# Optimization experiments

Hardware: AMD Instinct MI355X
Metric: run time of the kernel (lower is better)

The kernel has to match this reference:

```python
import jax, jax.numpy as jnp
import numpy as np

N_NODES = 2_000_000
E = 1_000_000
MEM = 32      # memory_dim
MSG = 32      # message_dim
EMB = 32      # embed_dim
EDGE = 2      # edge_dim


def _linear_params(key, out_dim, in_dim):
    kw, kb = jax.random.split(key)
    bound = 1.0 / np.sqrt(in_dim)
    W = jax.random.uniform(kw, (out_dim, in_dim), jnp.float32, -bound, bound)
    b = jax.random.uniform(kb, (out_dim,), jnp.float32, -bound, bound)
    return W, b


def setup_inputs() -> dict:
    key = jax.random.key(0)
    ks = jax.random.split(key, 16)
    inp = {}
    inp["src_ids"] = jax.random.randint(ks[0], (E,), 0, N_NODES)
    inp["dst_ids"] = jax.random.randint(ks[1], (E,), 0, N_NODES)
    inp["edge_feat"] = jax.random.normal(ks[2], (E, EDGE), jnp.float32)
    inp["delta_t"] = jax.random.uniform(ks[3], (E, 1), jnp.float32)
    # persistent node memory (torch init is zeros; use randn for a non-trivial baseline)
    inp["memory"] = jax.random.normal(ks[4], (N_NODES, MEM), jnp.float32) * 0.1
    # MessageFunction MLP: (2*MEM + EDGE + 1) -> MSG -> MSG
    inp["msg_W1"], inp["msg_b1"] = _linear_params(ks[5], MSG, 2 * MEM + EDGE + 1)
    inp["msg_W2"], inp["msg_b2"] = _linear_params(ks[6], MSG, MSG)
    # GRUCell(MSG, MEM): weight_ih [3*MEM, MSG], weight_hh [3*MEM, MEM]
    inp["gru_w_ih"], inp["gru_b_ih"] = _linear_params(ks[7], 3 * MEM, MSG)
    inp["gru_w_hh"], inp["gru_b_hh"] = _linear_params(ks[8], 3 * MEM, MEM)
    # MultiheadAttention with seq_len=1: only V and out projections affect output
    inp["attn_Wv"], inp["attn_bv"] = _linear_params(ks[9], MEM, MEM)
    inp["attn_Wo"], inp["attn_bo"] = _linear_params(ks[10], MEM, MEM)
    # TemporalEmbedding MLP: (MEM + EDGE) -> EMB -> EMB
    inp["emb_W1"], inp["emb_b1"] = _linear_params(ks[11], EMB, MEM + EDGE)
    inp["emb_W2"], inp["emb_b2"] = _linear_params(ks[12], EMB, EMB)
    # AnomalyClassifier: EMB -> 32 -> 1
    inp["cls_W1"], inp["cls_b1"] = _linear_params(ks[13], 32, EMB)
    inp["cls_W2"], inp["cls_b2"] = _linear_params(ks[14], 1, 32)
    return inp


def reference(src_ids, dst_ids, edge_feat, delta_t, memory,
              msg_W1, msg_b1, msg_W2, msg_b2,
              gru_w_ih, gru_w_hh, gru_b_ih, gru_b_hh,
              attn_Wv, attn_bv, attn_Wo, attn_bo,
              emb_W1, emb_b1, emb_W2, emb_b2,
              cls_W1, cls_b1, cls_W2, cls_b2):
    # gather per-node memory  [E, MEM]
    src_mem = memory[src_ids]
    dst_mem = memory[dst_ids]

    # MessageFunction: concat + 2-layer MLP
    x = jnp.concatenate([src_mem, dst_mem, edge_feat, delta_t], axis=-1)  # [E, 67]
    h = jax.nn.relu(x @ msg_W1.T + msg_b1)
    msg = h @ msg_W2.T + msg_b2  # [E, MSG]

    # GRUCell update on dst memory (torch gate order: r, z, n)
    gi = msg @ gru_w_ih.T + gru_b_ih      # [E, 3*MEM]
    gh = dst_mem @ gru_w_hh.T + gru_b_hh  # [E, 3*MEM]
    i_r, i_z, i_n = jnp.split(gi, 3, axis=-1)
    h_r, h_z, h_n = jnp.split(gh, 3, axis=-1)
    r = jax.nn.sigmoid(i_r + h_r)
    z = jax.nn.sigmoid(i_z + h_z)
    n = jnp.tanh(i_n + r * h_n)
    updated = (1.0 - z) * n + z * dst_mem  # [E, MEM]
    # scatter back into persistent buffer (detached in the torch module)
    new_memory = memory.at[dst_ids].set(jax.lax.stop_gradient(updated))

    # TemporalEmbedding: self-attention over a length-1 sequence. softmax of a
    # single score is exactly 1, so attn_out == out_proj(v_proj(dst_mem)).
    attn_out = (dst_mem @ attn_Wv.T + attn_bv) @ attn_Wo.T + attn_bo  # [E, MEM]
    e = jnp.concatenate([attn_out, edge_feat], axis=-1)  # [E, MEM+EDGE]
    embed = jax.nn.relu(e @ emb_W1.T + emb_b1) @ emb_W2.T + emb_b2  # [E, EMB]

    # AnomalyClassifier (dropout is identity at eval)
    logits = jax.nn.relu(embed @ cls_W1.T + cls_b1) @ cls_W2.T + cls_b2  # [E, 1]
    probs = jax.nn.sigmoid(logits).squeeze(-1)  # [E]
    return probs, new_memory
```

## Files before the change

### kernel.cpp

```cpp
#include <hip/hip_runtime.h>
#include <hip/hip_bf16.h>

typedef float  f32x4v __attribute__((ext_vector_type(4)));
typedef short  bf16x8 __attribute__((ext_vector_type(8)));

#define NFRAG   26
#define TB_F32  512
#define FRG_U16 (NFRAG*512)
#define SHARE_BYTES (TB_F32*4 + FRG_U16*2)
#define SHARE_U4 (SHARE_BYTES/16)
#define WC_OFF 7168

#define BLK 256
#define COPY_BLOCKS 256
#define EDGE_BLOCKS 1024
#define GRID (COPY_BLOCKS + EDGE_BLOCKS)
#define EDGE_WAVES (EDGE_BLOCKS * 4)

#define MFMA(a,b,c) __builtin_amdgcn_mfma_f32_16x16x32_bf16(a,b,c,0,0,0)

__device__ __forceinline__ float sigf(float v) { return 1.0f / (1.0f + __expf(-v)); }
__device__ __forceinline__ float tanhf_fast(float v) {
    float a = fabsf(v);
    float t = __expf(-2.0f * a);
    float r = (1.0f - t) / (1.0f + t);
    return v < 0.0f ? -r : r;
}
__device__ __forceinline__ unsigned pk(float a, float b) {
    union { __hip_bfloat162 h; unsigned u; } c;
    c.h = __float22bfloat162_rn(make_float2(a, b));
    return c.u;
}

union FragU { uint4 u4; bf16x8 s8; unsigned u[4]; };

__device__ __forceinline__ bf16x8 ldfrag(const unsigned short* frg, int idx_u16) {
    FragU c; c.u4 = *(const uint4*)(frg + idx_u16); return c.s8;
}
__device__ __forceinline__ f32x4v tbl(const float* tb, int idx_f32) {
    return *(const f32x4v*)(tb + idx_f32);
}
__device__ __forceinline__ bf16x8 relayout_reg(f32x4v h0, f32x4v h1) {
    FragU c;
    c.u[0] = pk(h0[0], h0[1]); c.u[1] = pk(h0[2], h0[3]);
    c.u[2] = pk(h1[0], h1[1]); c.u[3] = pk(h1[2], h1[3]);
    return c.s8;
}

__global__ void winner_k(const int* __restrict__ dst_ids, int* __restrict__ winner, int E) {
    int e = blockIdx.x * 256 + threadIdx.x;
    if (e < E) atomicMax(winner + dst_ids[e], e + 1);
}

__global__ void prep_k(const float* __restrict__ msg_W1, const float* __restrict__ msg_b1,
                       const float* __restrict__ msg_W2, const float* __restrict__ msg_b2,
                       const float* __restrict__ w_ih, const float* __restrict__ b_ih,
                       const float* __restrict__ w_hh, const float* __restrict__ b_hh,
                       const float* __restrict__ Wv, const float* __restrict__ bv,
                       const float* __restrict__ Wo, const float* __restrict__ bo,
                       const float* __restrict__ emb_W1, const float* __restrict__ emb_b1,
                       const float* __restrict__ emb_W2, const float* __restrict__ emb_b2,
                       const float* __restrict__ cls_W1, const float* __restrict__ cls_b1,
                       const float* __restrict__ cls_W2, float* __restrict__ WSf) {
    int t = threadIdx.x;
    float* tb = WSf;
    unsigned short* frg = (unsigned short*)(WSf + TB_F32);
    float* WC = WSf + WC_OFF;
    if (t < 32) {
        int j = t;
        tb[0*32+j]  = msg_b1[j];
        tb[1*32+j]  = msg_W1[j*67+64];
        tb[2*32+j]  = msg_W1[j*67+65];
        tb[3*32+j]  = msg_W1[j*67+66];
        tb[4*32+j]  = msg_b2[j];
        tb[5*32+j]  = b_ih[32+j] + b_hh[32+j];
        tb[6*32+j]  = b_ih[j] + b_hh[j];
        tb[7*32+j]  = b_hh[64+j];
        tb[8*32+j]  = b_ih[64+j];
        float a = bo[j];
        for (int o = 0; o < 32; ++o) a += Wo[j*32+o] * bv[o];
        tb[9*32+j]  = a;
        tb[10*32+j] = emb_b1[j];
        tb[11*32+j] = emb_W1[j*34+32];
        tb[12*32+j] = emb_W1[j*34+33];
        tb[13*32+j] = emb_b2[j];
        tb[14*32+j] = cls_b1[j];
        tb[15*32+j] = cls_W2[j];
    }
    for (int i = t; i < 1024; i += 256) {
        int j = i >> 5, k = i & 31;
        float a = 0.0f;
        for (int o = 0; o < 32; ++o) a += Wo[j*32+o] * Wv[o*32+k];
        WC[i] = a;
    }
    __syncthreads();
    for (int idx = t; idx < NFRAG * 512; idx += 256) {
        int f = idx >> 9, l = (idx >> 3) & 63, i = idx & 7;
        int r = l & 15, kb = ((l >> 4) << 3) + i;
        const float* P; int j0 = 0, k0 = 0, ld = 32;
        bool mapped = false;
        switch (f) {
            case 0:  P = msg_W1; j0 = 0;  k0 = 0;  ld = 67; break;
            case 1:  P = msg_W1; j0 = 0;  k0 = 32; ld = 67; break;
            case 2:  P = msg_W1; j0 = 16; k0 = 0;  ld = 67; break;
            case 3:  P = msg_W1; j0 = 16; k0 = 32; ld = 67; break;
            case 4:  P = msg_W2; j0 = 0;  mapped = true; break;
            case 5:  P = msg_W2; j0 = 16; mapped = true; break;
            case 6:  P = w_ih;   j0 = 32; mapped = true; break;
            case 7:  P = w_hh;   j0 = 32; break;
            case 8:  P = w_ih;   j0 = 48; mapped = true; break;
            case 9:  P = w_hh;   j0 = 48; break;
            case 10: P = w_ih;   j0 = 0;  mapped = true; break;
            case 11: P = w_hh;   j0 = 0;  break;
            case 12: P = w_ih;   j0 = 16; mapped = true; break;
            case 13: P = w_hh;   j0 = 16; break;
            case 14: P = w_hh;   j0 = 64; break;
            case 15: P = w_hh;   j0 = 80; break;
            case 16: P = w_ih;   j0 = 64; mapped = true; break;
            case 17: P = w_ih;   j0 = 80; mapped = true; break;
            case 18: P = WC;     j0 = 0;  break;
            case 19: P = WC;     j0 = 16; break;
            case 20: P = emb_W1; j0 = 0;  ld = 34; mapped = true; break;
            case 21: P = emb_W1; j0 = 16; ld = 34; mapped = true; break;
            case 22: P = emb_W2; j0 = 0;  mapped = true; break;
            case 23: P = emb_W2; j0 = 16; mapped = true; break;
            case 24: P = cls_W1; j0 = 0;  mapped = true; break;
            default: P = cls_W1; j0 = 16; mapped = true; break;
        }
        int kidx = kb;
        if (mapped) kidx = 16 * ((kb >> 2) & 1) + 4 * (kb >> 3) + (kb & 3);
        __hip_bfloat16 hv = __float2bfloat16(P[(j0 + r) * ld + k0 + kidx]);
        frg[idx] = *(unsigned short*)&hv;
    }
}

__device__ __forceinline__ void compute16(
    int grp, int E, int eI, int g, int lane,
    int e, int dst, int winv, float2 ef, float dtv,
    f32x4v sa, f32x4v sb, f32x4v da, f32x4v db, f32x4v t0, f32x4v t1,
    const float* tb, const unsigned short* frg, float clsb2,
    float* __restrict__ probs, float* __restrict__ out_mem) {
    int ob = 0, tbo = 0;
    asm volatile("" : "+v"(ob), "+v"(tbo));

    FragU Bs, Bd;
    Bs.u[0] = pk(sa[0], sa[1]); Bs.u[1] = pk(sa[2], sa[3]);
    Bs.u[2] = pk(sb[0], sb[1]); Bs.u[3] = pk(sb[2], sb[3]);
    Bd.u[0] = pk(da[0], da[1]); Bd.u[1] = pk(da[2], da[3]);
    Bd.u[2] = pk(db[0], db[1]); Bd.u[3] = pk(db[2], db[3]);
    f32x4v dmt[2]; dmt[0] = t0; dmt[1] = t1;

    f32x4v h[2];
#pragma unroll
    for (int jt = 0; jt < 2; ++jt) {
        f32x4v b1v = tbl(tb, 0*32 + jt*16 + 4*g + tbo);
        f32x4v w64 = tbl(tb, 1*32 + jt*16 + 4*g + tbo);
        f32x4v w65 = tbl(tb, 2*32 + jt*16 + 4*g + tbo);
        f32x4v w66 = tbl(tb, 3*32 + jt*16 + 4*g + tbo);
        f32x4v c;
#pragma unroll
        for (int i = 0; i < 4; ++i)
            c[i] = b1v[i] + ef.x * w64[i] + ef.y * w65[i] + dtv * w66[i];
        c = MFMA(ldfrag(frg, (jt*2+1)*512 + lane*8 + ob), Bd.s8, c);
        c = MFMA(ldfrag(frg, (jt*2+0)*512 + lane*8 + ob), Bs.s8, c);
#pragma unroll
        for (int i = 0; i < 4; ++i) c[i] = fmaxf(c[i], 0.0f);
        h[jt] = c;
    }
    bf16x8 Bh = relayout_reg(h[0], h[1]);

    f32x4v m[2];
#pragma unroll
    for (int jt = 0; jt < 2; ++jt)
        m[jt] = MFMA(ldfrag(frg, (4+jt)*512 + lane*8 + ob), Bh,
                     tbl(tb, 4*32 + jt*16 + 4*g + tbo));
    bf16x8 Bm = relayout_reg(m[0], m[1]);

    f32x4v zz[2], uu[2];
#pragma unroll
    for (int jt = 0; jt < 2; ++jt) {
        f32x4v c = tbl(tb, 5*32 + jt*16 + 4*g + tbo);
        c = MFMA(ldfrag(frg, (7+2*jt)*512 + lane*8 + ob), Bd.s8, c);
        c = MFMA(ldfrag(frg, (6+2*jt)*512 + lane*8 + ob), Bm, c);
#pragma unroll
        for (int i = 0; i < 4; ++i) c[i] = sigf(c[i]);
        zz[jt] = c;
    }
#pragma unroll
    for (int jt = 0; jt < 2; ++jt) {
        f32x4v c = tbl(tb, 6*32 + jt*16 + 4*g + tbo);
        c = MFMA(ldfrag(frg, (11+2*jt)*512 + lane*8 + ob), Bd.s8, c);
        c = MFMA(ldfrag(frg, (10+2*jt)*512 + lane*8 + ob), Bm, c);
        f32x4v hn = tbl(tb, 7*32 + jt*16 + 4*g + tbo);
        hn = MFMA(ldfrag(frg, (14+jt)*512 + lane*8 + ob), Bd.s8, hn);
        f32x4v bin = tbl(tb, 8*32 + jt*16 + 4*g + tbo);
        f32x4v npre;
#pragma unroll
        for (int i = 0; i < 4; ++i) npre[i] = fmaf(sigf(c[i]), hn[i], bin[i]);
        npre = MFMA(ldfrag(frg, (16+jt)*512 + lane*8 + ob), Bm, npre);
#pragma unroll
        for (int i = 0; i < 4; ++i) {
            float n = tanhf_fast(npre[i]);
            uu[jt][i] = n + zz[jt][i] * (dmt[jt][i] - n);
        }
    }
    if (winv == e + 1) {
        f32x4v* orow = (f32x4v*)(out_mem + (size_t)dst * 32);
        orow[g]     = uu[0];
        orow[4 + g] = uu[1];
    }

    f32x4v at[2];
#pragma unroll
    for (int jt = 0; jt < 2; ++jt)
        at[jt] = MFMA(ldfrag(frg, (18+jt)*512 + lane*8 + ob), Bd.s8,
                      tbl(tb, 9*32 + jt*16 + 4*g + tbo));
    bf16x8 Ba = relayout_reg(at[0], at[1]);
    f32x4v e1v[2];
#pragma unroll
    for (int jt = 0; jt < 2; ++jt) {
        f32x4v b  = tbl(tb, 10*32 + jt*16 + 4*g + tbo);
        f32x4v wa = tbl(tb, 11*32 + jt*16 + 4*g + tbo);
        f32x4v wb = tbl(tb, 12*32 + jt*16 + 4*g + tbo);
        f32x4v c;
#pragma unroll
        for (int i = 0; i < 4; ++i) c[i] = b[i] + ef.x * wa[i] + ef.y * wb[i];
        c = MFMA(ldfrag(frg, (20+jt)*512 + lane*8 + ob), Ba, c);
#pragma unroll
        for (int i = 0; i < 4; ++i) c[i] = fmaxf(c[i], 0.0f);
        e1v[jt] = c;
    }
    bf16x8 B1 = relayout_reg(e1v[0], e1v[1]);
    f32x4v e2v[2];
#pragma unroll
    for (int jt = 0; jt < 2; ++jt)
        e2v[jt] = MFMA(ldfrag(frg, (22+jt)*512 + lane*8 + ob), B1,
                       tbl(tb, 13*32 + jt*16 + 4*g + tbo));
    bf16x8 B2 = relayout_reg(e2v[0], e2v[1]);
    float part = 0.0f;
#pragma unroll
    for (int jt = 0; jt < 2; ++jt) {
        f32x4v c = MFMA(ldfrag(frg, (24+jt)*512 + lane*8 + ob), B2,
                        tbl(tb, 14*32 + jt*16 + 4*g + tbo));
        f32x4v w2 = tbl(tb, 15*32 + jt*16 + 4*g + tbo);
#pragma unroll
        for (int i = 0; i < 4; ++i) part = fmaf(fmaxf(c[i], 0.0f), w2[i], part);
    }
    part += __shfl_xor(part, 16);
    part += __shfl_xor(part, 32);
    if (lane < 16) {
        int ee = grp * 16 + eI;
        if (ee < E) probs[ee] = sigf(part + clsb2);
    }
}

__global__ __launch_bounds__(BLK, 5) void tgn_mfma16(
    const int* __restrict__ src_ids, const int* __restrict__ dst_ids,
    const float* __restrict__ edge_feat, const float* __restrict__ delta_t,
    const float* __restrict__ memory, const float* __restrict__ cls_b2,
    const float* __restrict__ WSf, const int* __restrict__ winner,
    float* __restrict__ probs, float* __restrict__ out_mem,
    int E, int N, int ngrp) {
    __shared__ uint4 sbuf[SHARE_U4];
    int bid = blockIdx.x, tid = threadIdx.x;

    if (bid < COPY_BLOCKS) {
        const f32x4v* m4 = (const f32x4v*)memory;
        f32x4v* o4 = (f32x4v*)out_mem;
        const long S = (long)COPY_BLOCKS * BLK;
        const long total4 = (long)N * 8;
        long i0 = (long)bid * BLK + tid;
        for (; i0 + 3 * S < total4; i0 += 4 * S) {
            long i1 = i0 + S, i2 = i0 + 2 * S, i3 = i0 + 3 * S;
            int w0 = winner[i0 >> 3];
            int w1 = winner[i1 >> 3];
            int w2 = winner[i2 >> 3];
            int w3 = winner[i3 >> 3];
            if (w0 == 0) o4[i0] = m4[i0];
            if (w1 == 0) o4[i1] = m4[i1];
            if (w2 == 0) o4[i2] = m4[i2];
            if (w3 == 0) o4[i3] = m4[i3];
        }
        for (; i0 < total4; i0 += S) {
            if (winner[i0 >> 3] == 0) o4[i0] = m4[i0];
        }
        return;
    }

    {
        const uint4* s = (const uint4*)WSf;
        for (int i = tid; i < SHARE_U4; i += BLK) sbuf[i] = s[i];
    }
    __syncthreads();
    const float* tb = (const float*)sbuf;
    const unsigned short* frg = (const unsigned short*)((const float*)sbuf + TB_F32);
    int wv = tid >> 6, lane = tid & 63;
    int eI = lane & 15, g = lane >> 4;
    int ewid = (bid - COPY_BLOCKS) * 4 + wv;
    float clsb2 = cls_b2[0];

#define PREF(P, G) do {                                                              \
    int ee = (G) * 16 + eI; if (ee >= E) ee = E - 1;                                 \
    e##P = ee;                                                                       \
    int sid = src_ids[ee]; dst##P = dst_ids[ee];                                     \
    ef##P = ((const float2*)edge_feat)[ee]; dt##P = delta_t[ee];                     \
    win##P = winner[dst##P];                                                         \
    const f32x4v* sp_ = (const f32x4v*)(memory + (size_t)sid * 32);                  \
    const f32x4v* dp_ = (const f32x4v*)(memory + (size_t)dst##P * 32);               \
    S##P##a = sp_[2*g]; S##P##b = sp_[2*g+1];                                        \
    D##P##a = dp_[2*g]; D##P##b = dp_[2*g+1];                                        \
    T##P##0 = dp_[g];   T##P##1 = dp_[4+g];                                          \
} while (0)

    int g0 = ewid;
    if (g0 < ngrp) {
        int eA, dstA, winA; float2 efA; float dtA;
        f32x4v SAa, SAb, DAa, DAb, TA0, TA1;
        int eB, dstB, winB; float2 efB; float dtB;
        f32x4v SBa, SBb, DBa, DBb, TB0, TB1;
        PREF(A, g0);
        for (;;) {
            int gn = g0 + EDGE_WAVES;
            { int gp = (gn < ngrp) ? gn : (ngrp - 1); PREF(B, gp); }
            asm volatile("" ::: "memory");
            compute16(g0, E, eI, g, lane, eA, dstA, winA, efA, dtA,
                      SAa, SAb, DAa, DAb, TA0, TA1,
                      tb, frg, clsb2, probs, out_mem);
            if (gn >= ngrp) break;
            g0 = gn;
            gn = g0 + EDGE_WAVES;
            { int gp = (gn < ngrp) ? gn : (ngrp - 1); PREF(A, gp); }
            asm volatile("" ::: "memory");
            compute16(g0, E, eI, g, lane, eB, dstB, winB, efB, dtB,
                      SBa, SBb, DBa, DBb, TB0, TB1,
                      tb, frg, clsb2, probs, out_mem);
            if (gn >= ngrp) break;
            g0 = gn;
        }
    }
#undef PREF
}

extern "C" void kernel_launch(void* const* d_in, const int* in_sizes, int n_in,
                              void* d_out, int out_size, void* d_ws, size_t ws_size,
                              hipStream_t stream) {
    const int*   src_ids   = (const int*)d_in[0];
    const int*   dst_ids   = (const int*)d_in[1];
    const float* edge_feat = (const float*)d_in[2];
    const float* delta_t   = (const float*)d_in[3];
    const float* memory    = (const float*)d_in[4];
    const float* msg_W1 = (const float*)d_in[5],  *msg_b1 = (const float*)d_in[6];
    const float* msg_W2 = (const float*)d_in[7],  *msg_b2 = (const float*)d_in[8];
    const float* w_ih   = (const float*)d_in[9],  *b_ih   = (const float*)d_in[10];
    const float* w_hh   = (const float*)d_in[11], *b_hh   = (const float*)d_in[12];
    const float* Wv     = (const float*)d_in[13], *bv     = (const float*)d_in[14];
    const float* Wo     = (const float*)d_in[15], *bo     = (const float*)d_in[16];
    const float* emb_W1 = (const float*)d_in[17], *emb_b1 = (const float*)d_in[18];
    const float* emb_W2 = (const float*)d_in[19], *emb_b2 = (const float*)d_in[20];
    const float* cls_W1 = (const float*)d_in[21], *cls_b1 = (const float*)d_in[22];
    const float* cls_W2 = (const float*)d_in[23], *cls_b2 = (const float*)d_in[24];

    int E = in_sizes[0];
    int N = in_sizes[4] / 32;
    int ngrp = (E + 15) / 16;

    int*   winner = (int*)d_ws;
    float* WSf    = (float*)((char*)d_ws + (size_t)N * sizeof(int));
    float* probs  = (float*)d_out;
    float* outmem = probs + E;

    hipMemsetAsync(winner, 0, (size_t)N * sizeof(int), stream);
    winner_k<<<(E + 255) / 256, 256, 0, stream>>>(dst_ids, winner, E);
    prep_k<<<1, 256, 0, stream>>>(msg_W1, msg_b1, msg_W2, msg_b2,
                                  w_ih, b_ih, w_hh, b_hh,
                                  Wv, bv, Wo, bo,
                                  emb_W1, emb_b1, emb_W2, emb_b2,
                                  cls_W1, cls_b1, cls_W2, WSf);
    tgn_mfma16<<<GRID, BLK, 0, stream>>>(src_ids, dst_ids, edge_feat, delta_t,
                                         memory, cls_b2, WSf, winner,
                                         probs, outmem, E, N, ngrp);
}
```

Before: 298.8 us.

## Interleave independent MFMA chains, split weight prep, use fast reciprocals

The per-tile compute is reordered so the GRU, attention/embedding and classifier MFMA chains are interleaved, letting independent matrix ops hide each other's latency. Weight-fragment packing moves into a separate kernel with one block per fragment instead of a single block. Sigmoid and tanh divisions become hardware reciprocals. Edge block count and launch-bounds occupancy are lowered, which gives more registers per thread but fewer waves to hide memory latency.

After: 279.4 us. 6.5% less time.

```diff
diff --git a/kernel.cpp b/kernel.cpp
--- a/kernel.cpp
+++ b/kernel.cpp
@@ -13,17 +13,19 @@
 
 #define BLK 256
 #define COPY_BLOCKS 256
-#define EDGE_BLOCKS 1024
+#define EDGE_BLOCKS 768
 #define GRID (COPY_BLOCKS + EDGE_BLOCKS)
 #define EDGE_WAVES (EDGE_BLOCKS * 4)
 
 #define MFMA(a,b,c) __builtin_amdgcn_mfma_f32_16x16x32_bf16(a,b,c,0,0,0)
 
-__device__ __forceinline__ float sigf(float v) { return 1.0f / (1.0f + __expf(-v)); }
+__device__ __forceinline__ float sigf(float v) {
+    return __builtin_amdgcn_rcpf(1.0f + __expf(-v));
+}
 __device__ __forceinline__ float tanhf_fast(float v) {
     float a = fabsf(v);
     float t = __expf(-2.0f * a);
-    float r = (1.0f - t) / (1.0f + t);
+    float r = (1.0f - t) * __builtin_amdgcn_rcpf(1.0f + t);
     return v < 0.0f ? -r : r;
 }
 __device__ __forceinline__ unsigned pk(float a, float b) {
@@ -52,19 +54,17 @@
     if (e < E) atomicMax(winner + dst_ids[e], e + 1);
 }
 
-__global__ void prep_k(const float* __restrict__ msg_W1, const float* __restrict__ msg_b1,
-                       const float* __restrict__ msg_W2, const float* __restrict__ msg_b2,
-                       const float* __restrict__ w_ih, const float* __restrict__ b_ih,
-                       const float* __restrict__ w_hh, const float* __restrict__ b_hh,
-                       const float* __restrict__ Wv, const float* __restrict__ bv,
-                       const float* __restrict__ Wo, const float* __restrict__ bo,
-                       const float* __restrict__ emb_W1, const float* __restrict__ emb_b1,
-                       const float* __restrict__ emb_W2, const float* __restrict__ emb_b2,
-                       const float* __restrict__ cls_W1, const float* __restrict__ cls_b1,
-                       const float* __restrict__ cls_W2, float* __restrict__ WSf) {
+__global__ void prep_wc_k(const float* __restrict__ msg_W1, const float* __restrict__ msg_b1,
+                          const float* __restrict__ msg_b2,
+                          const float* __restrict__ b_ih, const float* __restrict__ b_hh,
+                          const float* __restrict__ Wv, const float* __restrict__ bv,
+                          const float* __restrict__ Wo, const float* __restrict__ bo,
+                          const float* __restrict__ emb_W1, const float* __restrict__ emb_b1,
+                          const float* __restrict__ emb_b2,
+                          const float* __restrict__ cls_b1, const float* __restrict__ cls_W2,
+                          float* __restrict__ WSf) {
     int t = threadIdx.x;
     float* tb = WSf;
-    unsigned short* frg = (unsigned short*)(WSf + TB_F32);
     float* WC = WSf + WC_OFF;
     if (t < 32) {
         int j = t;
@@ -93,9 +93,21 @@
         for (int o = 0; o < 32; ++o) a += Wo[j*32+o] * Wv[o*32+k];
         WC[i] = a;
     }
-    __syncthreads();
-    for (int idx = t; idx < NFRAG * 512; idx += 256) {
-        int f = idx >> 9, l = (idx >> 3) & 63, i = idx & 7;
+}
+
+__global__ void prep_frag_k(const float* __restrict__ msg_W1,
+                            const float* __restrict__ msg_W2,
+                            const float* __restrict__ w_ih,
+                            const float* __restrict__ w_hh,
+                            const float* __restrict__ emb_W1,
+                            const float* __restrict__ emb_W2,
+                            const float* __restrict__ cls_W1,
+                            float* __restrict__ WSf) {
+    int f = blockIdx.x;
+    unsigned short* frg = (unsigned short*)(WSf + TB_F32);
+    const float* WC = WSf + WC_OFF;
+    for (int k2 = threadIdx.x; k2 < 512; k2 += 256) {
+        int l = k2 >> 3, i = k2 & 7;
         int r = l & 15, kb = ((l >> 4) << 3) + i;
         const float* P; int j0 = 0, k0 = 0, ld = 32;
         bool mapped = false;
@@ -130,7 +142,7 @@
         int kidx = kb;
         if (mapped) kidx = 16 * ((kb >> 2) & 1) + 4 * (kb >> 3) + (kb & 3);
         __hip_bfloat16 hv = __float2bfloat16(P[(j0 + r) * ld + k0 + kidx]);
-        frg[idx] = *(unsigned short*)&hv;
+        frg[f * 512 + k2] = *(unsigned short*)&hv;
     }
 }
 
@@ -143,108 +155,98 @@
     int ob = 0, tbo = 0;
     asm volatile("" : "+v"(ob), "+v"(tbo));
 
+#define LFX(f) ldfrag(frg, (f) * 512 + lane * 8 + ob)
+#define TBX(t_, jt_) tbl(tb, (t_) * 32 + (jt_) * 16 + 4 * g + tbo)
+
     FragU Bs, Bd;
     Bs.u[0] = pk(sa[0], sa[1]); Bs.u[1] = pk(sa[2], sa[3]);
     Bs.u[2] = pk(sb[0], sb[1]); Bs.u[3] = pk(sb[2], sb[3]);
     Bd.u[0] = pk(da[0], da[1]); Bd.u[1] = pk(da[2], da[3]);
     Bd.u[2] = pk(db[0], db[1]); Bd.u[3] = pk(db[2], db[3]);
-    f32x4v dmt[2]; dmt[0] = t0; dmt[1] = t1;
-
-    f32x4v h[2];
-#pragma unroll
-    for (int jt = 0; jt < 2; ++jt) {
-        f32x4v b1v = tbl(tb, 0*32 + jt*16 + 4*g + tbo);
-        f32x4v w64 = tbl(tb, 1*32 + jt*16 + 4*g + tbo);
-        f32x4v w65 = tbl(tb, 2*32 + jt*16 + 4*g + tbo);
-        f32x4v w66 = tbl(tb, 3*32 + jt*16 + 4*g + tbo);
-        f32x4v c;
-#pragma unroll
-        for (int i = 0; i < 4; ++i)
-            c[i] = b1v[i] + ef.x * w64[i] + ef.y * w65[i] + dtv * w66[i];
-        c = MFMA(ldfrag(frg, (jt*2+1)*512 + lane*8 + ob), Bd.s8, c);
-        c = MFMA(ldfrag(frg, (jt*2+0)*512 + lane*8 + ob), Bs.s8, c);
-#pragma unroll
-        for (int i = 0; i < 4; ++i) c[i] = fmaxf(c[i], 0.0f);
-        h[jt] = c;
-    }
-    bf16x8 Bh = relayout_reg(h[0], h[1]);
-
-    f32x4v m[2];
-#pragma unroll
-    for (int jt = 0; jt < 2; ++jt)
-        m[jt] = MFMA(ldfrag(frg, (4+jt)*512 + lane*8 + ob), Bh,
-                     tbl(tb, 4*32 + jt*16 + 4*g + tbo));
-    bf16x8 Bm = relayout_reg(m[0], m[1]);
-
-    f32x4v zz[2], uu[2];
-#pragma unroll
-    for (int jt = 0; jt < 2; ++jt) {
-        f32x4v c = tbl(tb, 5*32 + jt*16 + 4*g + tbo);
-        c = MFMA(ldfrag(frg, (7+2*jt)*512 + lane*8 + ob), Bd.s8, c);
-        c = MFMA(ldfrag(frg, (6+2*jt)*512 + lane*8 + ob), Bm, c);
-#pragma unroll
-        for (int i = 0; i < 4; ++i) c[i] = sigf(c[i]);
-        zz[jt] = c;
-    }
-#pragma unroll
-    for (int jt = 0; jt < 2; ++jt) {
-        f32x4v c = tbl(tb, 6*32 + jt*16 + 4*g + tbo);
-        c = MFMA(ldfrag(frg, (11+2*jt)*512 + lane*8 + ob), Bd.s8, c);
-        c = MFMA(ldfrag(frg, (10+2*jt)*512 + lane*8 + ob), Bm, c);
-        f32x4v hn = tbl(tb, 7*32 + jt*16 + 4*g + tbo);
-        hn = MFMA(ldfrag(frg, (14+jt)*512 + lane*8 + ob), Bd.s8, hn);
-        f32x4v bin = tbl(tb, 8*32 + jt*16 + 4*g + tbo);
-        f32x4v npre;
-#pragma unroll
-        for (int i = 0; i < 4; ++i) npre[i] = fmaf(sigf(c[i]), hn[i], bin[i]);
-        npre = MFMA(ldfrag(frg, (16+jt)*512 + lane*8 + ob), Bm, npre);
+    f32x4v dmt0 = t0, dmt1 = t1;
+
+    f32x4v h0, h1;
+    {
+        f32x4v b0 = TBX(0,0), wa0 = TBX(1,0), wb0 = TBX(2,0), wc0 = TBX(3,0);
+        f32x4v b1 = TBX(0,1), wa1 = TBX(1,1), wb1 = TBX(2,1), wc1 = TBX(3,1);
+        f32x4v c0, c1;
 #pragma unroll
         for (int i = 0; i < 4; ++i) {
-            float n = tanhf_fast(npre[i]);
-            uu[jt][i] = n + zz[jt][i] * (dmt[jt][i] - n);
-        }
+            c0[i] = b0[i] + ef.x * wa0[i] + ef.y * wb0[i] + dtv * wc0[i];
+            c1[i] = b1[i] + ef.x * wa1[i] + ef.y * wb1[i] + dtv * wc1[i];
+        }
+        c0 = MFMA(LFX(1), Bd.s8, c0); c0 = MFMA(LFX(0), Bs.s8, c0);
+        c1 = MFMA(LFX(3), Bd.s8, c1); c1 = MFMA(LFX(2), Bs.s8, c1);
+        h0 = c0; h1 = c1;
+    }
+    f32x4v at0 = MFMA(LFX(18), Bd.s8, TBX(9,0));
+    f32x4v at1 = MFMA(LFX(19), Bd.s8, TBX(9,1));
+#pragma unroll
+    for (int i = 0; i < 4; ++i) { h0[i] = fmaxf(h0[i], 0.0f); h1[i] = fmaxf(h1[i], 0.0f); }
+    bf16x8 Bh = relayout_reg(h0, h1);
+    f32x4v m0 = MFMA(LFX(4), Bh, TBX(4,0));
+    f32x4v m1 = MFMA(LFX(5), Bh, TBX(4,1));
+    bf16x8 Ba = relayout_reg(at0, at1);
+    f32x4v e10, e11;
+    {
+        f32x4v b0 = TBX(10,0), wa0 = TBX(11,0), wb0 = TBX(12,0);
+        f32x4v b1 = TBX(10,1), wa1 = TBX(11,1), wb1 = TBX(12,1);
+        f32x4v c0, c1;
+#pragma unroll
+        for (int i = 0; i < 4; ++i) {
+            c0[i] = b0[i] + ef.x * wa0[i] + ef.y * wb0[i];
+            c1[i] = b1[i] + ef.x * wa1[i] + ef.y * wb1[i];
+        }
+        e10 = MFMA(LFX(20), Ba, c0);
+        e11 = MFMA(LFX(21), Ba, c1);
+    }
+    bf16x8 Bm = relayout_reg(m0, m1);
+    f32x4v z0 = TBX(5,0); z0 = MFMA(LFX(7), Bd.s8, z0); z0 = MFMA(LFX(6), Bm, z0);
+    f32x4v z1 = TBX(5,1); z1 = MFMA(LFX(9), Bd.s8, z1); z1 = MFMA(LFX(8), Bm, z1);
+#pragma unroll
+    for (int i = 0; i < 4; ++i) { e10[i] = fmaxf(e10[i], 0.0f); e11[i] = fmaxf(e11[i], 0.0f); }
+    bf16x8 B1 = relayout_reg(e10, e11);
+    f32x4v e20 = MFMA(LFX(22), B1, TBX(13,0));
+    f32x4v e21 = MFMA(LFX(23), B1, TBX(13,1));
+#pragma unroll
+    for (int i = 0; i < 4; ++i) { z0[i] = sigf(z0[i]); z1[i] = sigf(z1[i]); }
+    f32x4v r0 = TBX(6,0); r0 = MFMA(LFX(11), Bd.s8, r0); r0 = MFMA(LFX(10), Bm, r0);
+    f32x4v r1 = TBX(6,1); r1 = MFMA(LFX(13), Bd.s8, r1); r1 = MFMA(LFX(12), Bm, r1);
+    f32x4v hn0 = TBX(7,0); hn0 = MFMA(LFX(14), Bd.s8, hn0);
+    f32x4v hn1 = TBX(7,1); hn1 = MFMA(LFX(15), Bd.s8, hn1);
+    bf16x8 B2 = relayout_reg(e20, e21);
+    f32x4v cc0 = MFMA(LFX(24), B2, TBX(14,0));
+    f32x4v cc1 = MFMA(LFX(25), B2, TBX(14,1));
+    f32x4v bin0 = TBX(8,0), bin1 = TBX(8,1);
+    f32x4v np0, np1;
+#pragma unroll
+    for (int i = 0; i < 4; ++i) {
+        np0[i] = fmaf(sigf(r0[i]), hn0[i], bin0[i]);
+        np1[i] = fmaf(sigf(r1[i]), hn1[i], bin1[i]);
+    }
+    np0 = MFMA(LFX(16), Bm, np0);
+    np1 = MFMA(LFX(17), Bm, np1);
+    float part = 0.0f;
+    {
+        f32x4v w20 = TBX(15,0), w21 = TBX(15,1);
+#pragma unroll
+        for (int i = 0; i < 4; ++i) {
+            part = fmaf(fmaxf(cc0[i], 0.0f), w20[i], part);
+            part = fmaf(fmaxf(cc1[i], 0.0f), w21[i], part);
+        }
+    }
+    f32x4v u0, u1;
+#pragma unroll
+    for (int i = 0; i < 4; ++i) {
+        float n0 = tanhf_fast(np0[i]);
+        float n1 = tanhf_fast(np1[i]);
+        u0[i] = n0 + z0[i] * (dmt0[i] - n0);
+        u1[i] = n1 + z1[i] * (dmt1[i] - n1);
     }
     if (winv == e + 1) {
         f32x4v* orow = (f32x4v*)(out_mem + (size_t)dst * 32);
-        orow[g]     = uu[0];
-        orow[4 + g] = uu[1];
-    }
-
-    f32x4v at[2];
-#pragma unroll
-    for (int jt = 0; jt < 2; ++jt)
-        at[jt] = MFMA(ldfrag(frg, (18+jt)*512 + lane*8 + ob), Bd.s8,
-                      tbl(tb, 9*32 + jt*16 + 4*g + tbo));
-    bf16x8 Ba = relayout_reg(at[0], at[1]);
-    f32x4v e1v[2];
-#pragma unroll
-    for (int jt = 0; jt < 2; ++jt) {
-        f32x4v b  = tbl(tb, 10*32 + jt*16 + 4*g + tbo);
-        f32x4v wa = tbl(tb, 11*32 + jt*16 + 4*g + tbo);
-        f32x4v wb = tbl(tb, 12*32 + jt*16 + 4*g + tbo);
-        f32x4v c;
-#pragma unroll
-        for (int i = 0; i < 4; ++i) c[i] = b[i] + ef.x * wa[i] + ef.y * wb[i];
-        c = MFMA(ldfrag(frg, (20+jt)*512 + lane*8 + ob), Ba, c);
-#pragma unroll
-        for (int i = 0; i < 4; ++i) c[i] = fmaxf(c[i], 0.0f);
-        e1v[jt] = c;
-    }
-    bf16x8 B1 = relayout_reg(e1v[0], e1v[1]);
-    f32x4v e2v[2];
-#pragma unroll
-    for (int jt = 0; jt < 2; ++jt)
-        e2v[jt] = MFMA(ldfrag(frg, (22+jt)*512 + lane*8 + ob), B1,
-                       tbl(tb, 13*32 + jt*16 + 4*g + tbo));
-    bf16x8 B2 = relayout_reg(e2v[0], e2v[1]);
-    float part = 0.0f;
-#pragma unroll
-    for (int jt = 0; jt < 2; ++jt) {
-        f32x4v c = MFMA(ldfrag(frg, (24+jt)*512 + lane*8 + ob), B2,
-                        tbl(tb, 14*32 + jt*16 + 4*g + tbo));
-        f32x4v w2 = tbl(tb, 15*32 + jt*16 + 4*g + tbo);
-#pragma unroll
-        for (int i = 0; i < 4; ++i) part = fmaf(fmaxf(c[i], 0.0f), w2[i], part);
+        orow[g]     = u0;
+        orow[4 + g] = u1;
     }
     part += __shfl_xor(part, 16);
     part += __shfl_xor(part, 32);
@@ -252,9 +254,11 @@
         int ee = grp * 16 + eI;
         if (ee < E) probs[ee] = sigf(part + clsb2);
     }
-}
-
-__global__ __launch_bounds__(BLK, 5) void tgn_mfma16(
+#undef LFX
+#undef TBX
+}
+
+__global__ __launch_bounds__(BLK, 4) void tgn_mfma16(
     const int* __restrict__ src_ids, const int* __restrict__ dst_ids,
     const float* __restrict__ edge_feat, const float* __restrict__ delta_t,
     const float* __restrict__ memory, const float* __restrict__ cls_b2,
@@ -371,11 +375,11 @@
 
     hipMemsetAsync(winner, 0, (size_t)N * sizeof(int), stream);
     winner_k<<<(E + 255) / 256, 256, 0, stream>>>(dst_ids, winner, E);
-    prep_k<<<1, 256, 0, stream>>>(msg_W1, msg_b1, msg_W2, msg_b2,
-                                  w_ih, b_ih, w_hh, b_hh,
-                                  Wv, bv, Wo, bo,
-                                  emb_W1, emb_b1, emb_W2, emb_b2,
-                                  cls_W1, cls_b1, cls_W2, WSf);
+    prep_wc_k<<<1, 256, 0, stream>>>(msg_W1, msg_b1, msg_b2, b_ih, b_hh,
+                                     Wv, bv, Wo, bo, emb_W1, emb_b1, emb_b2,
+                                     cls_b1, cls_W2, WSf);
+    prep_frag_k<<<NFRAG, 256, 0, stream>>>(msg_W1, msg_W2, w_ih, w_hh,
+                                           emb_W1, emb_W2, cls_W1, WSf);
     tgn_mfma16<<<GRID, BLK, 0, stream>>>(src_ids, dst_ids, edge_feat, delta_t,
                                          memory, cls_b2, WSf, winner,
                                          probs, outmem, E, N, ngrp);
```
